# Performance work log

Measured on AMD Instinct MI355X. Metric: run time of the kernel, lower is better.

The kernel has to match this reference:

```python
import jax, jax.numpy as jnp
import numpy as np

D = 1024      # model dim
H = 16        # heads
DH = 64       # dim per head (lucidrains default)
DEPTH = 6
MLP = 2048
P = 32
PD = 3 * P * P   # 3072
NC = 1000
B = 4         # packed sequences
N = 640       # tokens per packed sequence (incl. padding)
M = 18        # images per packed sequence
GRID = 8      # image_size // patch_size
SIZES = [(8,8),(8,8),(7,7),(7,7),(6,8),(8,6),(6,6),(5,7),(7,5),(5,5),(4,8),(8,4),(4,6),(6,4),(4,4),(3,5),(5,3),(3,3)]
SCALE = DH ** -0.5


def _pack_meta():
    hs, ws, ids = [], [], []
    for i, (h, w) in enumerate(SIZES):
        hh, ww = np.meshgrid(np.arange(h), np.arange(w), indexing='ij')
        hs.append(hh.ravel()); ws.append(ww.ravel()); ids.append(np.full(h * w, i))
    h = np.concatenate(hs); w = np.concatenate(ws); ii = np.concatenate(ids)
    pad = N - h.shape[0]
    h = np.pad(h, (0, pad)); w = np.pad(w, (0, pad))
    ii = np.pad(ii, (0, pad), constant_values=-1)  # padding tokens form their own block
    return (np.tile(h, (B, 1)).astype(np.int32),
            np.tile(w, (B, 1)).astype(np.int32),
            np.tile(ii, (B, 1)).astype(np.int32))


def _ln(x, g, b, eps=1e-5):
    m = x.mean(-1, keepdims=True)
    v = ((x - m) ** 2).mean(-1, keepdims=True)
    return (x - m) * jax.lax.rsqrt(v + eps) * g + b


def _heads(t):  # [b, n, H*DH] -> [b, H, n, DH]
    return t.reshape(t.shape[0], t.shape[1], H, DH).swapaxes(1, 2)


def _mha(q_in, kv_in, mask, Wq, Wkv, Wo, qn_g, qn_b, kn_g, kn_b):
    # NaViT attention: pre-norm applied by caller to q_in; per-head qk LayerNorm; no biases.
    q = _ln(_heads(q_in @ Wq), qn_g, qn_b)
    k, v = jnp.split(kv_in @ Wkv, 2, axis=-1)
    k = _ln(_heads(k), kn_g, kn_b)
    v = _heads(v)
    dots = jnp.einsum('bhid,bhjd->bhij', q, k) * SCALE
    dots = jnp.where(mask, dots, jnp.finfo(dots.dtype).min)
    o = jnp.einsum('bhij,bhjd->bhid', jax.nn.softmax(dots, axis=-1), v)
    o = o.swapaxes(1, 2).reshape(o.shape[0], -1, H * DH)
    return o @ Wo


def _forward(patches, pe_ln1_g, pe_ln1_b, W_pe, b_pe, pe_ln2_g, pe_ln2_b, pos_h, pos_w,
             ln1_g, ln1_b, qn_g, qn_b, kn_g, kn_b, Wq, Wkv, Wo, ln2_g, ln2_b,
             W1, b1, W2, b2, fin_g, fin_b, pool_q, pl_ln_g, pl_ln_b, pl_qn_g, pl_qn_b,
             pl_kn_g, pl_kn_b, pl_Wq, pl_Wkv, pl_Wo, head_g, head_b, W_head, b_head,
             h_idx, w_idx, image_ids):
    # patch embedding: LN -> Linear -> LN, then factorized 2D pos embed
    x = _ln(patches, pe_ln1_g, pe_ln1_b) @ W_pe + b_pe
    x = _ln(x, pe_ln2_g, pe_ln2_b)
    x = x + pos_h[h_idx] + pos_w[w_idx]
    # block-diagonal attention mask: tokens attend only within their own image
    blk = (image_ids[:, :, None] == image_ids[:, None, :])[:, None]  # [B,1,N,N]
    for l in range(DEPTH):
        xn = _ln(x, ln1_g[l], ln1_b[l])
        x = x + _mha(xn, xn, blk, Wq[l], Wkv[l], Wo[l], qn_g[l], qn_b[l], kn_g[l], kn_b[l])
        xn = _ln(x, ln2_g[l], ln2_b[l])
        x = x + jax.nn.gelu(xn @ W1[l] + b1[l], approximate=False) @ W2[l] + b2[l]
    x = _ln(x, fin_g, fin_b)
    # attention pooling: one learned query per packed image (context NOT re-normed, as in na_vit)
    queries = jnp.broadcast_to(pool_q, (B, M, D))
    qn = _ln(queries, pl_ln_g, pl_ln_b)
    pmask = (jnp.arange(M)[None, :, None] == image_ids[:, None, :])[:, None]  # [B,1,M,N]
    pooled = _mha(qn, x, pmask, pl_Wq, pl_Wkv, pl_Wo, pl_qn_g, pl_qn_b, pl_kn_g, pl_kn_b) + queries
    pooled = pooled.reshape(B * M, D)
    return _ln(pooled, head_g, head_b) @ W_head + b_head  # [B*M, 1000]


def setup_inputs() -> dict:
    key = jax.random.key(0)
    ks = iter(jax.random.split(key, 32))
    h_idx, w_idx, image_ids = _pack_meta()
    f32 = jnp.float32
    d = dict(
        patches=jax.random.normal(next(ks), (B, N, PD), f32),
        pe_ln1_g=jnp.ones((PD,), f32), pe_ln1_b=jnp.zeros((PD,), f32),
        W_pe=0.02 * jax.random.normal(next(ks), (PD, D), f32), b_pe=jnp.zeros((D,), f32),
        pe_ln2_g=jnp.ones((D,), f32), pe_ln2_b=jnp.zeros((D,), f32),
        pos_h=0.02 * jax.random.normal(next(ks), (GRID, D), f32),
        pos_w=0.02 * jax.random.normal(next(ks), (GRID, D), f32),
        ln1_g=jnp.ones((DEPTH, D), f32), ln1_b=jnp.zeros((DEPTH, D), f32),
        qn_g=jnp.ones((DEPTH, DH), f32), qn_b=jnp.zeros((DEPTH, DH), f32),
        kn_g=jnp.ones((DEPTH, DH), f32), kn_b=jnp.zeros((DEPTH, DH), f32),
        Wq=0.02 * jax.random.normal(next(ks), (DEPTH, D, H * DH), f32),
        Wkv=0.02 * jax.random.normal(next(ks), (DEPTH, D, 2 * H * DH), f32),
        Wo=0.02 * jax.random.normal(next(ks), (DEPTH, H * DH, D), f32),
        ln2_g=jnp.ones((DEPTH, D), f32), ln2_b=jnp.zeros((DEPTH, D), f32),
        W1=0.02 * jax.random.normal(next(ks), (DEPTH, D, MLP), f32), b1=jnp.zeros((DEPTH, MLP), f32),
        W2=0.02 * jax.random.normal(next(ks), (DEPTH, MLP, D), f32), b2=jnp.zeros((DEPTH, D), f32),
        fin_g=jnp.ones((D,), f32), fin_b=jnp.zeros((D,), f32),
        pool_q=0.02 * jax.random.normal(next(ks), (D,), f32),
        pl_ln_g=jnp.ones((D,), f32), pl_ln_b=jnp.zeros((D,), f32),
        pl_qn_g=jnp.ones((DH,), f32), pl_qn_b=jnp.zeros((DH,), f32),
        pl_kn_g=jnp.ones((DH,), f32), pl_kn_b=jnp.zeros((DH,), f32),
        pl_Wq=0.02 * jax.random.normal(next(ks), (D, H * DH), f32),
        pl_Wkv=0.02 * jax.random.normal(next(ks), (D, 2 * H * DH), f32),
        pl_Wo=0.02 * jax.random.normal(next(ks), (H * DH, D), f32),
        head_g=jnp.ones((D,), f32), head_b=jnp.zeros((D,), f32),
        W_head=0.02 * jax.random.normal(next(ks), (D, NC), f32), b_head=jnp.zeros((NC,), f32),
        h_idx=jnp.asarray(h_idx), w_idx=jnp.asarray(w_idx), image_ids=jnp.asarray(image_ids),
    )
    return d


def reference(patches, pe_ln1_g, pe_ln1_b, W_pe, b_pe, pe_ln2_g, pe_ln2_b, pos_h, pos_w,
              ln1_g, ln1_b, qn_g, qn_b, kn_g, kn_b, Wq, Wkv, Wo, ln2_g, ln2_b,
              W1, b1, W2, b2, fin_g, fin_b, pool_q, pl_ln_g, pl_ln_b, pl_qn_g, pl_qn_b,
              pl_kn_g, pl_kn_b, pl_Wq, pl_Wkv, pl_Wo, head_g, head_b, W_head, b_head,
              h_idx, w_idx, image_ids):
    return _forward(patches, pe_ln1_g, pe_ln1_b, W_pe, b_pe, pe_ln2_g, pe_ln2_b, pos_h, pos_w,
                    ln1_g, ln1_b, qn_g, qn_b, kn_g, kn_b, Wq, Wkv, Wo, ln2_g, ln2_b,
                    W1, b1, W2, b2, fin_g, fin_b, pool_q, pl_ln_g, pl_ln_b, pl_qn_g, pl_qn_b,
                    pl_kn_g, pl_kn_b, pl_Wq, pl_Wkv, pl_Wo, head_g, head_b, W_head, b_head,
                    h_idx, w_idx, image_ids)
```

## Files before the change

kernel.cpp:

```cpp
#include <hip/hip_runtime.h>
#include <cmath>

constexpr int kB = 4, kN = 640, kD = 1024, kH = 16, kDH = 64;
constexpr int kDepth = 6, kMLP = 2048, kPD = 3072, kNC = 1000, kM = 18;
constexpr float kScale = 0.125f;
constexpr float kNegInf = -3.4028235e38f;

typedef __bf16 bf16;
typedef __attribute__((ext_vector_type(8))) __bf16 bf16x8;
typedef __attribute__((ext_vector_type(4))) __bf16 bf16x4;
typedef __attribute__((ext_vector_type(4))) float f32x4;

#define AS1 __attribute__((address_space(1)))
#define AS3 __attribute__((address_space(3)))

__device__ __forceinline__ void gload16(const void* g, void* l) {
  __builtin_amdgcn_global_load_lds((AS1 void*)g, (AS3 void*)l, 16, 0, 0);
}

constexpr size_t kMEG = 1048576;
constexpr size_t kOffPe = 0;
constexpr size_t kLayer0 = 3 * kMEG;
constexpr size_t kLayerSz = 8 * kMEG;
constexpr size_t kOffPool = kLayer0 + 6 * kLayerSz;
constexpr size_t kOffPlWq = kOffPool;
constexpr size_t kOffPlWkv = kOffPool + 1 * kMEG;
constexpr size_t kOffPlWo = kOffPool + 3 * kMEG;
constexpr size_t kOffHead = kOffPool + 4 * kMEG;

__global__ __launch_bounds__(256) void wt_all_kernel(
    const float* __restrict__ pe, const float* __restrict__ wq,
    const float* __restrict__ wkv, const float* __restrict__ wo,
    const float* __restrict__ w1, const float* __restrict__ w2,
    const float* __restrict__ plq, const float* __restrict__ plkv,
    const float* __restrict__ plo, const float* __restrict__ whead,
    bf16* __restrict__ WTB) {
  const int j = blockIdx.y;
  const float* W;
  size_t doff;
  int K, Nc, Np;
  if (j == 0) {
    W = pe; K = 3072; Nc = 1024; Np = 1024; doff = kOffPe;
  } else if (j < 31) {
    const int l = (j - 1) / 5, w = (j - 1) % 5;
    const size_t lbase = kLayer0 + (size_t)l * kLayerSz;
    switch (w) {
      case 0:  W = wq  + (size_t)l * kMEG;     K = 1024; Nc = 1024; doff = lbase;            break;
      case 1:  W = wkv + (size_t)l * 2 * kMEG; K = 1024; Nc = 2048; doff = lbase + kMEG;     break;
      case 2:  W = wo  + (size_t)l * kMEG;     K = 1024; Nc = 1024; doff = lbase + 3 * kMEG; break;
      case 3:  W = w1  + (size_t)l * 2 * kMEG; K = 1024; Nc = 2048; doff = lbase + 4 * kMEG; break;
      default: W = w2  + (size_t)l * 2 * kMEG; K = 2048; Nc = 1024; doff = lbase + 6 * kMEG; break;
    }
    Np = Nc;
  } else if (j == 31) { W = plq;  K = 1024; Nc = 1024; Np = 1024; doff = kOffPlWq; }
  else if (j == 32)   { W = plkv; K = 1024; Nc = 2048; Np = 2048; doff = kOffPlWkv; }
  else if (j == 33)   { W = plo;  K = 1024; Nc = 1024; Np = 1024; doff = kOffPlWo; }
  else                { W = whead; K = 1024; Nc = 1000; Np = 1024; doff = kOffHead; }
  const int nb = Np >> 10;
  const int ntiles = nb * (K >> 6);
  const int tile = blockIdx.x;
  if (tile >= ntiles) return;
  const int n0 = (tile % nb) * 1024 + threadIdx.x * 4;
  const int k0 = (tile / nb) * 64;
  const bool inb = (n0 + 3 < Nc);
  bf16* WT = WTB + doff;
#pragma unroll
  for (int ch = 0; ch < 4; ++ch) {
    float4 v[16];
    if (inb) {
      const float* src = W + (size_t)(k0 + ch * 16) * Nc + n0;
#pragma unroll
      for (int i = 0; i < 16; ++i)
        v[i] = *(const float4*)(src + (size_t)i * Nc);
    } else {
#pragma unroll
      for (int i = 0; i < 16; ++i) v[i] = float4{0.f, 0.f, 0.f, 0.f};
    }
#pragma unroll
    for (int c = 0; c < 4; ++c) {
      bf16x8 lo, hi;
#pragma unroll
      for (int i = 0; i < 8; ++i) {
        lo[i] = (bf16)((&v[i].x)[c]);
        hi[i] = (bf16)((&v[i + 8].x)[c]);
      }
      bf16* d = WT + (size_t)(n0 + c) * K + k0 + ch * 16;
      *(bf16x8*)(d) = lo;
      *(bf16x8*)(d + 8) = hi;
    }
  }
}

__global__ __launch_bounds__(64) void span_kernel(
    const int* __restrict__ ids, int2* __restrict__ spans) {
  const int img = blockIdx.x, b = blockIdx.y;
  const int want = (img < kM) ? img : -1;
  int lo = kN, hi = -1;
  for (int j = threadIdx.x; j < kN; j += 64) {
    if (ids[b * kN + j] == want) { lo = min(lo, j); hi = max(hi, j); }
  }
#pragma unroll
  for (int off = 32; off; off >>= 1) {
    lo = min(lo, __shfl_xor(lo, off));
    hi = max(hi, __shfl_xor(hi, off));
  }
  if (threadIdx.x == 0) spans[b * (kM + 1) + img] = make_int2(lo, hi);
}

template <typename OT>
__global__ __launch_bounds__(256) void ln_kernel(
    const float* __restrict__ in, OT* __restrict__ out,
    const float* __restrict__ g, const float* __restrict__ b, int K) {
  const int row = blockIdx.x;
  const float* x = in + (size_t)row * K;
  OT* o = out + (size_t)row * K;
  const int K4 = K >> 2;
  float s = 0.f, s2 = 0.f;
  for (int c = threadIdx.x; c < K4; c += 256) {
    const float4 v = ((const float4*)x)[c];
    s += v.x + v.y + v.z + v.w;
    s2 += v.x * v.x + v.y * v.y + v.z * v.z + v.w * v.w;
  }
#pragma unroll
  for (int off = 32; off; off >>= 1) { s += __shfl_down(s, off); s2 += __shfl_down(s2, off); }
  __shared__ float ls[4], ls2[4];
  __shared__ float sm, sr;
  const int wid = threadIdx.x >> 6, lane = threadIdx.x & 63;
  if (lane == 0) { ls[wid] = s; ls2[wid] = s2; }
  __syncthreads();
  if (threadIdx.x == 0) {
    float a = ls[0] + ls[1] + ls[2] + ls[3];
    float a2 = ls2[0] + ls2[1] + ls2[2] + ls2[3];
    float mean = a / K;
    float var = a2 / K - mean * mean;
    sm = mean; sr = rsqrtf(var + 1e-5f);
  }
  __syncthreads();
  const float mean = sm, r = sr;
  for (int c = threadIdx.x; c < K4; c += 256) {
    const float4 v = ((const float4*)x)[c];
    const float4 gv = ((const float4*)g)[c];
    const float4 bv = ((const float4*)b)[c];
    const int d = c * 4;
    o[d + 0] = (OT)((v.x - mean) * r * gv.x + bv.x);
    o[d + 1] = (OT)((v.y - mean) * r * gv.y + bv.y);
    o[d + 2] = (OT)((v.z - mean) * r * gv.z + bv.z);
    o[d + 3] = (OT)((v.w - mean) * r * gv.w + bv.w);
  }
}

__global__ __launch_bounds__(256) void ln_pos_kernel(
    const float* __restrict__ in, float* __restrict__ out,
    const float* __restrict__ g, const float* __restrict__ b,
    const float* __restrict__ ph, const float* __restrict__ pw,
    const int* __restrict__ hi, const int* __restrict__ wi) {
  const int row = blockIdx.x;
  const float* x = in + (size_t)row * kD;
  float* o = out + (size_t)row * kD;
  const int c = threadIdx.x;
  const float4 v = ((const float4*)x)[c];
  float s = v.x + v.y + v.z + v.w;
  float s2 = v.x * v.x + v.y * v.y + v.z * v.z + v.w * v.w;
#pragma unroll
  for (int off = 32; off; off >>= 1) { s += __shfl_down(s, off); s2 += __shfl_down(s2, off); }
  __shared__ float ls[4], ls2[4];
  __shared__ float sm, sr;
  const int wid = threadIdx.x >> 6, lane = threadIdx.x & 63;
  if (lane == 0) { ls[wid] = s; ls2[wid] = s2; }
  __syncthreads();
  if (threadIdx.x == 0) {
    float a = ls[0] + ls[1] + ls[2] + ls[3];
    float a2 = ls2[0] + ls2[1] + ls2[2] + ls2[3];
    float mean = a / kD;
    float var = a2 / kD - mean * mean;
    sm = mean; sr = rsqrtf(var + 1e-5f);
  }
  __syncthreads();
  const float mean = sm, r = sr;
  const float4* phr = (const float4*)(ph + (size_t)hi[row] * kD);
  const float4* pwr = (const float4*)(pw + (size_t)wi[row] * kD);
  const float4 gv = ((const float4*)g)[c];
  const float4 bv = ((const float4*)b)[c];
  const float4 hv = phr[c], wv = pwr[c];
  float4 ov;
  ov.x = (v.x - mean) * r * gv.x + bv.x + hv.x + wv.x;
  ov.y = (v.y - mean) * r * gv.y + bv.y + hv.y + wv.y;
  ov.z = (v.z - mean) * r * gv.z + bv.z + hv.z + wv.z;
  ov.w = (v.w - mean) * r * gv.w + bv.w + hv.w + wv.w;
  ((float4*)o)[c] = ov;
}

__global__ __launch_bounds__(256) void poolq_kernel(
    const float* __restrict__ pq, const float* __restrict__ lg,
    const float* __restrict__ lb, const bf16* __restrict__ WqT,
    const float* __restrict__ qg, const float* __restrict__ qb,
    float* __restrict__ qpool) {
  const int h = blockIdx.x, tid = threadIdx.x;
  __shared__ float qs[1024];
  __shared__ float red[256];
  __shared__ float ls[4], ls2[4];
  __shared__ float sm, sr;
  const float4 v = ((const float4*)pq)[tid];
  float s = v.x + v.y + v.z + v.w;
  float s2 = v.x * v.x + v.y * v.y + v.z * v.z + v.w * v.w;
#pragma unroll
  for (int off = 32; off; off >>= 1) { s += __shfl_down(s, off); s2 += __shfl_down(s2, off); }
  const int wid = tid >> 6, lane = tid & 63;
  if (lane == 0) { ls[wid] = s; ls2[wid] = s2; }
  __syncthreads();
  if (tid == 0) {
    float a = ls[0] + ls[1] + ls[2] + ls[3];
    float a2 = ls2[0] + ls2[1] + ls2[2] + ls2[3];
    float mean = a / kD;
    sm = mean; sr = rsqrtf(a2 / kD - mean * mean + 1e-5f);
  }
  __syncthreads();
  {
    const float mean = sm, r = sr;
    const float4 gv = ((const float4*)lg)[tid];
    const float4 bv = ((const float4*)lb)[tid];
    qs[tid * 4 + 0] = (v.x - mean) * r * gv.x + bv.x;
    qs[tid * 4 + 1] = (v.y - mean) * r * gv.y + bv.y;
    qs[tid * 4 + 2] = (v.z - mean) * r * gv.z + bv.z;
    qs[tid * 4 + 3] = (v.w - mean) * r * gv.w + bv.w;
  }
  __syncthreads();
  const int d = tid & 63, qq = tid >> 6;
  const bf16* wrow = WqT + (size_t)(h * 64 + d) * 1024 + qq * 256;
  const float* qp = qs + qq * 256;
  float part = 0.f;
  for (int k = 0; k < 256; k += 8) {
    const bf16x8 w8 = *(const bf16x8*)(wrow + k);
#pragma unroll
    for (int e = 0; e < 8; ++e) part += qp[k + e] * (float)w8[e];
  }
  red[tid] = part;
  __syncthreads();
  if (tid < 64) {
    const float dot = red[tid] + red[tid + 64] + red[tid + 128] + red[tid + 192];
    float hs = dot, hs2 = dot * dot;
#pragma unroll
    for (int off = 32; off; off >>= 1) { hs += __shfl_xor(hs, off); hs2 += __shfl_xor(hs2, off); }
    const float m = hs * (1.f / kDH);
    const float r = rsqrtf(hs2 * (1.f / kDH) - m * m + 1e-5f);
    qpool[h * 64 + tid] = (dot - m) * r * qg[tid] + qb[tid];
  }
}

template <int NI, bool OUT_BF, bool GELU, bool HLN>
__global__ __launch_bounds__(256) void gemm64_kernel(
    const bf16* __restrict__ A, const bf16* __restrict__ WT,
    float* __restrict__ Cf, bf16* __restrict__ Cb,
    const float* __restrict__ bias, const float* __restrict__ res,
    const float* __restrict__ hg, const float* __restrict__ hb,
    int K, int Ncol, int nbx) {
  constexpr int BN = NI * 32;
  __shared__ __align__(16) bf16 As[2][64 * 64];
  __shared__ __align__(16) bf16 Bs[2][BN * 64];
  const int tid = threadIdx.x, lane = tid & 63, wid = tid >> 6;
  const int wr = wid >> 1, wc = wid & 1;
  const int cpx = gridDim.x >> 3;
  const int swz = (blockIdx.x & 7) * cpx + (blockIdx.x >> 3);
  const int row0 = (swz / nbx) * 64, col0 = (swz % nbx) * BN;
  const int fr = lane & 15, fg = lane >> 4;
  f32x4 acc[2][NI] = {};
  bf16* sA = As[0]; bf16* sB = Bs[0];
  bf16* dA = As[1]; bf16* dB = Bs[1];

  auto stage = [&](bf16* tA, bf16* tB, int kt) {
#pragma unroll
    for (int i = 0; i < 2; ++i) {
      const int c = i * 256 + tid;
      const int r = c >> 3, ci = c & 7;
      gload16(A + (size_t)(row0 + r) * K + kt + ((ci ^ (r & 7)) * 8),
              tA + (i * 256 + wid * 64) * 8);
    }
#pragma unroll
    for (int i = 0; i < NI; ++i) {
      const int c = i * 256 + tid;
      const int r = c >> 3, ci = c & 7;
      gload16(WT + (size_t)(col0 + r) * K + kt + ((ci ^ (r & 7)) * 8),
              tB + (i * 256 + wid * 64) * 8);
    }
  };
  auto compute = [&](const bf16* tA, const bf16* tB) {
#pragma unroll
    for (int kk = 0; kk < 2; ++kk) {
      bf16x8 af[2], bfr[NI];
#pragma unroll
      for (int mi = 0; mi < 2; ++mi) {
        const int r = wr * 32 + mi * 16 + fr;
        af[mi] = *(const bf16x8*)(tA + r * 64 + (((kk * 4 + fg) ^ (r & 7)) * 8));
      }
#pragma unroll
      for (int ni = 0; ni < NI; ++ni) {
        const int r = wc * (NI * 16) + ni * 16 + fr;
        bfr[ni] = *(const bf16x8*)(tB + r * 64 + (((kk * 4 + fg) ^ (r & 7)) * 8));
      }
#pragma unroll
      for (int mi = 0; mi < 2; ++mi)
#pragma unroll
        for (int ni = 0; ni < NI; ++ni)
          acc[mi][ni] = __builtin_amdgcn_mfma_f32_16x16x32_bf16(af[mi], bfr[ni], acc[mi][ni], 0, 0, 0);
    }
  };

  const int NT = K >> 6;
  stage(sA, sB, 0);
  __syncthreads();
  for (int t = 1; t < NT; ++t) {
    stage(dA, dB, t * 64);
    compute(sA, sB);
    __syncthreads();
    bf16* u;
    u = sA; sA = dA; dA = u;
    u = sB; sB = dB; dB = u;
  }
  compute(sA, sB);

  const int rb = row0 + wr * 32 + fg * 4;
  const int cb = col0 + wc * (NI * 16) + fr;
  float hm[2][4], hr[2][4];
  if (HLN) {
#pragma unroll
    for (int mi = 0; mi < 2; ++mi)
#pragma unroll
      for (int r = 0; r < 4; ++r) {
        float s = 0.f, s2 = 0.f;
#pragma unroll
        for (int ni = 0; ni < NI; ++ni) {
          const float v = acc[mi][ni][r];
          s += v; s2 += v * v;
        }
#pragma unroll
        for (int off = 1; off < 16; off <<= 1) {
          s += __shfl_xor(s, off); s2 += __shfl_xor(s2, off);
        }
        const float m = s * (1.f / kDH);
        hm[mi][r] = m;
        hr[mi][r] = rsqrtf(s2 * (1.f / kDH) - m * m + 1e-5f);
      }
  }
  const bool kHalf = HLN && (cb < kD);
#pragma unroll
  for (int mi = 0; mi < 2; ++mi) {
#pragma unroll
    for (int ni = 0; ni < NI; ++ni) {
      const int cc = cb + ni * 16;
      const float bb = bias ? bias[cc] : 0.f;
      const float hgv = HLN ? hg[ni * 16 + fr] : 0.f;
      const float hbv = HLN ? hb[ni * 16 + fr] : 0.f;
#pragma unroll
      for (int r = 0; r < 4; ++r) {
        const int rr = rb + mi * 16 + r;
        float v = acc[mi][ni][r] + bb;
        if (res) v += res[(size_t)rr * Ncol + cc];
        if (GELU) v = 0.5f * v * (1.f + erff(v * 0.70710678118654752f));
        if (HLN && kHalf) v = (v - hm[mi][r]) * hr[mi][r] * hgv + hbv;
        if (OUT_BF) Cb[(size_t)rr * Ncol + cc] = (bf16)v;
        else        Cf[(size_t)rr * Ncol + cc] = v;
      }
    }
  }
}

template <bool OUT_BF>
__global__ __launch_bounds__(256) void gemm_tail_kernel(
    const bf16* __restrict__ A, const bf16* __restrict__ WT,
    float* __restrict__ Cf, bf16* __restrict__ Cb,
    const float* __restrict__ bias, const float* __restrict__ resv,
    int Mr, int K, int Nc, int ldc, int resmode) {
  __shared__ __align__(16) bf16 As[64][40];
  __shared__ __align__(16) bf16 Bs[128][40];
  const int tid = threadIdx.x;
  const int lane = tid & 63, wid = tid >> 6;
  const int row0 = blockIdx.y * 64, col0 = blockIdx.x * 128;
  f32x4 acc[4][2] = {};
  const int am = tid >> 2, ako = (tid & 3) * 8;
  const int fr = lane & 15, fg = (lane >> 4) * 8;
  for (int k0 = 0; k0 < K; k0 += 32) {
    if (row0 + am < Mr)
      *(bf16x8*)&As[am][ako] = *(const bf16x8*)(A + (size_t)(row0 + am) * K + k0 + ako);
    else {
      bf16x8 z = {};
      *(bf16x8*)&As[am][ako] = z;
    }
#pragma unroll
    for (int it = 0; it < 2; ++it) {
      const int c = it * 256 + tid;
      const int n = c >> 2, ko = (c & 3) * 8;
      *(bf16x8*)&Bs[n][ko] = *(const bf16x8*)(WT + (size_t)(col0 + n) * K + k0 + ko);
    }
    __syncthreads();
    bf16x8 af[4], bfr[2];
#pragma unroll
    for (int mi = 0; mi < 4; ++mi) af[mi] = *(const bf16x8*)&As[mi * 16 + fr][fg];
#pragma unroll
    for (int ni = 0; ni < 2; ++ni) bfr[ni] = *(const bf16x8*)&Bs[wid * 32 + ni * 16 + fr][fg];
#pragma unroll
    for (int mi = 0; mi < 4; ++mi)
#pragma unroll
      for (int ni = 0; ni < 2; ++ni)
        acc[mi][ni] = __builtin_amdgcn_mfma_f32_16x16x32_bf16(af[mi], bfr[ni], acc[mi][ni], 0, 0, 0);
    __syncthreads();
  }
  const int r4 = (lane >> 4) * 4;
  const int cc0 = col0 + wid * 32 + (lane & 15);
#pragma unroll
  for (int mi = 0; mi < 4; ++mi) {
#pragma unroll
    for (int ni = 0; ni < 2; ++ni) {
      const int cc = cc0 + ni * 16;
      if (cc >= Nc) continue;
#pragma unroll
      for (int r = 0; r < 4; ++r) {
        const int rr = row0 + mi * 16 + r4 + r;
        if (rr >= Mr) continue;
        float v = acc[mi][ni][r];
        if (bias) v += bias[cc];
        if (resmode == 1) v += resv[(size_t)rr * ldc + cc];
        else if (resmode == 2) v += resv[cc];
        if (OUT_BF) Cb[(size_t)rr * ldc + cc] = (bf16)v;
        else        Cf[(size_t)rr * ldc + cc] = v;
      }
    }
  }
}

__global__ __launch_bounds__(256) void attn_kernel(
    const bf16* __restrict__ qkv, const int2* __restrict__ spans,
    const float* __restrict__ qg, const float* __restrict__ qb,
    const float* __restrict__ kg, const float* __restrict__ kb,
    bf16* __restrict__ o) {
  const int h = blockIdx.x, img = blockIdx.y, b = blockIdx.z;
  const int tid = threadIdx.x, lane = tid & 63, wid = tid >> 6;
  __shared__ __align__(16) bf16 Qs[64][72];
  __shared__ __align__(16) bf16 Ks[64][72];
  __shared__ __align__(16) bf16 Vt[64][72];
  __shared__ __align__(16) bf16 Ps[64][72];
  const int2 sp = spans[b * (kM + 1) + img];
  if (sp.y < 0) return;
  const int start = sp.x, T = sp.y - sp.x + 1;
  if (img == kM) {
    for (int j = start + wid; j <= sp.y; j += 4)
      o[((size_t)(b * kN + j)) * kD + h * kDH + lane] = (bf16)0.f;
    return;
  }
#pragma unroll
  for (int it = 0; it < 2; ++it) {
    const int ch = it * 256 + tid;
    const int r = ch >> 3, d0 = (ch & 7) * 8;
    if (r < T) {
      const bf16* base = qkv + ((size_t)(b * kN + start + r)) * 3072 + h * kDH + d0;
      const bf16x8 qv = *(const bf16x8*)(base);
      const bf16x8 kv = *(const bf16x8*)(base + 1024);
      const bf16x8 vv = *(const bf16x8*)(base + 2048);
      float qf[8], kf[8];
      float sq = 0.f, sq2 = 0.f, sk = 0.f, sk2 = 0.f;
#pragma unroll
      for (int e = 0; e < 8; ++e) {
        qf[e] = (float)qv[e]; kf[e] = (float)kv[e];
        sq += qf[e]; sq2 += qf[e] * qf[e];
        sk += kf[e]; sk2 += kf[e] * kf[e];
      }
#pragma unroll
      for (int off = 1; off < 8; off <<= 1) {
        sq += __shfl_xor(sq, off); sq2 += __shfl_xor(sq2, off);
        sk += __shfl_xor(sk, off); sk2 += __shfl_xor(sk2, off);
      }
      const float qm = sq * (1.f / 64);
      const float qr = rsqrtf(sq2 * (1.f / 64) - qm * qm + 1e-5f);
      const float km = sk * (1.f / 64);
      const float kr = rsqrtf(sk2 * (1.f / 64) - km * km + 1e-5f);
      bf16x8 qw, kw;
#pragma unroll
      for (int e = 0; e < 8; ++e) {
        qw[e] = (bf16)((qf[e] - qm) * qr * qg[d0 + e] + qb[d0 + e]);
        kw[e] = (bf16)((kf[e] - km) * kr * kg[d0 + e] + kb[d0 + e]);
      }
      *(bf16x8*)&Qs[r][d0] = qw;
      *(bf16x8*)&Ks[r][d0] = kw;
#pragma unroll
      for (int e = 0; e < 8; ++e) Vt[d0 + e][r] = vv[e];
    } else {
      const bf16x8 z = {};
      *(bf16x8*)&Qs[r][d0] = z;
      *(bf16x8*)&Ks[r][d0] = z;
#pragma unroll
      for (int e = 0; e < 8; ++e) Vt[d0 + e][r] = (bf16)0.f;
    }
  }
  __syncthreads();
  const int fr = lane & 15, fg = lane >> 4;
  const int r0 = wid * 16;
  f32x4 sacc[4] = {};
#pragma unroll
  for (int k0 = 0; k0 < 64; k0 += 32) {
    const bf16x8 aq = *(const bf16x8*)&Qs[r0 + fr][k0 + fg * 8];
#pragma unroll
    for (int ni = 0; ni < 4; ++ni) {
      const bf16x8 bk = *(const bf16x8*)&Ks[ni * 16 + fr][k0 + fg * 8];
      sacc[ni] = __builtin_amdgcn_mfma_f32_16x16x32_bf16(aq, bk, sacc[ni], 0, 0, 0);
    }
  }
  float inv[4];
#pragma unroll
  for (int r = 0; r < 4; ++r) {
    float mx = kNegInf;
#pragma unroll
    for (int ni = 0; ni < 4; ++ni) {
      const float s = (ni * 16 + fr < T) ? sacc[ni][r] * kScale : kNegInf;
      sacc[ni][r] = s;
      mx = fmaxf(mx, s);
    }
#pragma unroll
    for (int off = 1; off < 16; off <<= 1) mx = fmaxf(mx, __shfl_xor(mx, off));
    float sum = 0.f;
#pragma unroll
    for (int ni = 0; ni < 4; ++ni) {
      const float p = __expf(sacc[ni][r] - mx);
      sacc[ni][r] = p;
      sum += p;
    }
#pragma unroll
    for (int off = 1; off < 16; off <<= 1) sum += __shfl_xor(sum, off);
    inv[r] = 1.f / sum;
  }
#pragma unroll
  for (int ni = 0; ni < 4; ++ni)
#pragma unroll
    for (int r = 0; r < 4; ++r)
      Ps[r0 + fg * 4 + r][ni * 16 + fr] = (bf16)sacc[ni][r];
  f32x4 oacc[4] = {};
#pragma unroll
  for (int k0 = 0; k0 < 64; k0 += 32) {
    const bf16x8 ap = *(const bf16x8*)&Ps[r0 + fr][k0 + fg * 8];
#pragma unroll
    for (int ni = 0; ni < 4; ++ni) {
      const bf16x8 bv = *(const bf16x8*)&Vt[ni * 16 + fr][k0 + fg * 8];
      oacc[ni] = __builtin_amdgcn_mfma_f32_16x16x32_bf16(ap, bv, oacc[ni], 0, 0, 0);
    }
  }
#pragma unroll
  for (int r = 0; r < 4; ++r) {
    const int i = r0 + fg * 4 + r;
    if (i < T) {
      const size_t orow = ((size_t)(b * kN + start + i)) * kD + h * kDH;
      const float iv = inv[r];
#pragma unroll
      for (int ni = 0; ni < 4; ++ni)
        o[orow + ni * 16 + fr] = (bf16)(oacc[ni][r] * iv);
    }
  }
}

__global__ __launch_bounds__(64) void poolattn_kernel(
    const float* __restrict__ qp, const bf16* __restrict__ kv,
    const int2* __restrict__ spans, bf16* __restrict__ o) {
  const int blk = blockIdx.x;
  const int h = blk % kH;
  const int bm = blk / kH;
  const int m = bm % kM, b = bm / kM;
  const int lane = threadIdx.x;
  __shared__ float sc[kN];
  __shared__ float qs[kDH];
  qs[lane] = qp[h * kDH + lane];
  __syncthreads();
  const int2 sp = spans[b * (kM + 1) + m];
  const int jlo = sp.x, jhi = sp.y + 1;
  float mymax = kNegInf;
  for (int j = jlo + lane; j < jhi; j += 64) {
    const bf16* krow = kv + ((size_t)(b * kN + j)) * (2 * kD) + h * kDH;
    float dot = 0.f;
#pragma unroll
    for (int d = 0; d < kDH; ++d) dot += qs[d] * (float)krow[d];
    const float s = dot * kScale;
    sc[j] = s;
    mymax = fmaxf(mymax, s);
  }
#pragma unroll
  for (int off = 32; off; off >>= 1) mymax = fmaxf(mymax, __shfl_xor(mymax, off));
  float mysum = 0.f;
  for (int j = jlo + lane; j < jhi; j += 64) {
    const float p = __expf(sc[j] - mymax);
    sc[j] = p;
    mysum += p;
  }
#pragma unroll
  for (int off = 32; off; off >>= 1) mysum += __shfl_xor(mysum, off);
  const float inv = 1.f / mysum;
  __syncthreads();
  float acc = 0.f;
  const bf16* vptr = kv + ((size_t)(b * kN + jlo)) * (2 * kD) + kD + h * kDH + lane;
  for (int j = jlo; j < jhi; ++j, vptr += 2 * kD) acc += sc[j] * (float)vptr[0];
  o[((size_t)(b * kM + m)) * kD + h * kDH + lane] = (bf16)(acc * inv);
}

extern "C" void kernel_launch(void* const* d_in, const int* in_sizes, int n_in,
                              void* d_out, int out_size, void* d_ws, size_t ws_size,
                              hipStream_t stream) {
  const float* patches  = (const float*)d_in[0];
  const float* pe_ln1_g = (const float*)d_in[1];
  const float* pe_ln1_b = (const float*)d_in[2];
  const float* W_pe     = (const float*)d_in[3];
  const float* b_pe     = (const float*)d_in[4];
  const float* pe_ln2_g = (const float*)d_in[5];
  const float* pe_ln2_b = (const float*)d_in[6];
  const float* pos_h    = (const float*)d_in[7];
  const float* pos_w    = (const float*)d_in[8];
  const float* ln1_g    = (const float*)d_in[9];
  const float* ln1_b    = (const float*)d_in[10];
  const float* qn_g     = (const float*)d_in[11];
  const float* qn_b     = (const float*)d_in[12];
  const float* kn_g     = (const float*)d_in[13];
  const float* kn_b     = (const float*)d_in[14];
  const float* Wq       = (const float*)d_in[15];
  const float* Wkv      = (const float*)d_in[16];
  const float* Wo       = (const float*)d_in[17];
  const float* ln2_g    = (const float*)d_in[18];
  const float* ln2_b    = (const float*)d_in[19];
  const float* W1       = (const float*)d_in[20];
  const float* b1       = (const float*)d_in[21];
  const float* W2       = (const float*)d_in[22];
  const float* b2       = (const float*)d_in[23];
  const float* fin_g    = (const float*)d_in[24];
  const float* fin_b    = (const float*)d_in[25];
  const float* pool_q   = (const float*)d_in[26];
  const float* pl_ln_g  = (const float*)d_in[27];
  const float* pl_ln_b  = (const float*)d_in[28];
  const float* pl_qn_g  = (const float*)d_in[29];
  const float* pl_qn_b  = (const float*)d_in[30];
  const float* pl_kn_g  = (const float*)d_in[31];
  const float* pl_kn_b  = (const float*)d_in[32];
  const float* pl_Wq    = (const float*)d_in[33];
  const float* pl_Wkv   = (const float*)d_in[34];
  const float* pl_Wo    = (const float*)d_in[35];
  const float* head_g   = (const float*)d_in[36];
  const float* head_b   = (const float*)d_in[37];
  const float* W_head   = (const float*)d_in[38];
  const float* b_head   = (const float*)d_in[39];
  const int* h_idx      = (const int*)d_in[40];
  const int* w_idx      = (const int*)d_in[41];
  const int* image_ids  = (const int*)d_in[42];
  float* out = (float*)d_out;

  const size_t SZ = (size_t)kB * kN * kD;
  char* p = (char*)d_ws;
  float* x    = (float*)p;           p += SZ * 4;
  bf16*  xnb  = (bf16*)p;            p += SZ * 2;
  char*  scratch = p;                p += 32u * 1024 * 1024;
  char*  smalls = p;                 p += 1u * 1024 * 1024;
  bf16*  wtbuf = (bf16*)p;
  bf16*  qkvbb = (bf16*)scratch;
  bf16*  attno = (bf16*)(scratch + 16u * 1024 * 1024);
  bf16*  plnb  = (bf16*)scratch;
  float* emb   = (float*)(scratch + 16u * 1024 * 1024);
  bf16*  h1b   = (bf16*)scratch;
  bf16*  kvpoolb = (bf16*)scratch;
  float* qpool   = (float*)smalls;
  bf16*  opoolb  = (bf16*)(smalls + 8192);
  float* pooled  = (float*)(smalls + 8192 + 163840);
  bf16*  pooledn = (bf16*)(smalls + 8192 + 163840 + 327680);
  int2*  spans   = (int2*)(smalls + 8192 + 163840 + 327680 + 163840);

  const int BN = kB * kN;
  const int nbyM = BN / 64;

  span_kernel<<<dim3(kM + 1, kB), 64, 0, stream>>>(image_ids, spans);
  wt_all_kernel<<<dim3(48, 35), 256, 0, stream>>>(
      W_pe, Wq, Wkv, Wo, W1, W2, pl_Wq, pl_Wkv, pl_Wo, W_head, wtbuf);

  ln_kernel<bf16><<<BN, 256, 0, stream>>>(patches, plnb, pe_ln1_g, pe_ln1_b, kPD);
  gemm64_kernel<2, false, false, false><<<(kD / 64) * nbyM, 256, 0, stream>>>(
      plnb, wtbuf + kOffPe, emb, nullptr, b_pe, nullptr, nullptr, nullptr, kPD, kD, kD / 64);
  ln_pos_kernel<<<BN, 256, 0, stream>>>(emb, x, pe_ln2_g, pe_ln2_b, pos_h, pos_w, h_idx, w_idx);

  for (int l = 0; l < kDepth; ++l) {
    const bf16* lw = wtbuf + kLayer0 + (size_t)l * kLayerSz;
    ln_kernel<bf16><<<BN, 256, 0, stream>>>(x, xnb, ln1_g + (size_t)l * kD, ln1_b + (size_t)l * kD, kD);
    gemm64_kernel<4, true, false, false><<<(3 * kD / 128) * nbyM, 256, 0, stream>>>(
        xnb, lw, nullptr, qkvbb, nullptr, nullptr, nullptr, nullptr, kD, 3 * kD, 3 * kD / 128);
    attn_kernel<<<dim3(kH, kM + 1, kB), 256, 0, stream>>>(
        qkvbb, spans,
        qn_g + (size_t)l * kDH, qn_b + (size_t)l * kDH,
        kn_g + (size_t)l * kDH, kn_b + (size_t)l * kDH, attno);
    gemm64_kernel<2, false, false, false><<<(kD / 64) * nbyM, 256, 0, stream>>>(
        attno, lw + 3 * kMEG, x, nullptr, nullptr, x, nullptr, nullptr, kD, kD, kD / 64);
    ln_kernel<bf16><<<BN, 256, 0, stream>>>(x, xnb, ln2_g + (size_t)l * kD, ln2_b + (size_t)l * kD, kD);
    gemm64_kernel<4, true, true, false><<<(kMLP / 128) * nbyM, 256, 0, stream>>>(
        xnb, lw + 4 * kMEG, nullptr, h1b, b1 + (size_t)l * kMLP, nullptr, nullptr, nullptr, kD, kMLP, kMLP / 128);
    gemm64_kernel<2, false, false, false><<<(kD / 64) * nbyM, 256, 0, stream>>>(
        h1b, lw + 6 * kMEG, x, nullptr, b2 + (size_t)l * kD, x, nullptr, nullptr, kMLP, kD, kD / 64);
  }

  ln_kernel<bf16><<<BN, 256, 0, stream>>>(x, xnb, fin_g, fin_b, kD);

  poolq_kernel<<<kH, 256, 0, stream>>>(
      pool_q, pl_ln_g, pl_ln_b, wtbuf + kOffPlWq, pl_qn_g, pl_qn_b, qpool);
  gemm64_kernel<4, true, false, true><<<(2 * kD / 128) * nbyM, 256, 0, stream>>>(
      xnb, wtbuf + kOffPlWkv, nullptr, kvpoolb, nullptr, nullptr, pl_kn_g, pl_kn_b, kD, 2 * kD, 2 * kD / 128);
  poolattn_kernel<<<kB * kM * kH, 64, 0, stream>>>(qpool, kvpoolb, spans, opoolb);
  gemm_tail_kernel<false><<<dim3(8, 2), 256, 0, stream>>>(
      opoolb, wtbuf + kOffPlWo, pooled, nullptr, nullptr, pool_q, kB * kM, kD, kD, kD, 2);

  ln_kernel<bf16><<<kB * kM, 256, 0, stream>>>(pooled, pooledn, head_g, head_b, kD);
  gemm_tail_kernel<false><<<dim3(8, 2), 256, 0, stream>>>(
      pooledn, wtbuf + kOffHead, out, nullptr, b_head, nullptr, kB * kM, kD, kNC, kNC, 0);
}
```

Before: 1.004 ms.

## Store residual stream in bf16 and retile weight transpose through LDS

The residual stream x moves from fp32 to bf16. The layernorm kernels read bf16 through a new ln_bf_kernel, and the residual GEMMs read and write bf16, which halves the traffic for the residual reads and writes. The weight-transpose kernel is also rewritten to use 64x64 tiles staged in padded shared memory, with many more blocks, so that both the global reads and the writes are coalesced. Accumulating the residual in bf16 across six layers reduces precision and may push the output past the accuracy tolerance.

```diff
diff --git a/kernel.cpp b/kernel.cpp
--- a/kernel.cpp
+++ b/kernel.cpp
@@ -56,38 +56,44 @@
   else if (j == 32)   { W = plkv; K = 1024; Nc = 2048; Np = 2048; doff = kOffPlWkv; }
   else if (j == 33)   { W = plo;  K = 1024; Nc = 1024; Np = 1024; doff = kOffPlWo; }
   else                { W = whead; K = 1024; Nc = 1000; Np = 1024; doff = kOffHead; }
-  const int nb = Np >> 10;
-  const int ntiles = nb * (K >> 6);
+  const int nbx = Np >> 6;
+  const int ntiles = nbx * (K >> 6);
   const int tile = blockIdx.x;
   if (tile >= ntiles) return;
-  const int n0 = (tile % nb) * 1024 + threadIdx.x * 4;
-  const int k0 = (tile / nb) * 64;
-  const bool inb = (n0 + 3 < Nc);
+  const int n0 = (tile % nbx) * 64, k0 = (tile / nbx) * 64;
   bf16* WT = WTB + doff;
-#pragma unroll
-  for (int ch = 0; ch < 4; ++ch) {
-    float4 v[16];
-    if (inb) {
-      const float* src = W + (size_t)(k0 + ch * 16) * Nc + n0;
-#pragma unroll
-      for (int i = 0; i < 16; ++i)
-        v[i] = *(const float4*)(src + (size_t)i * Nc);
-    } else {
-#pragma unroll
-      for (int i = 0; i < 16; ++i) v[i] = float4{0.f, 0.f, 0.f, 0.f};
-    }
-#pragma unroll
-    for (int c = 0; c < 4; ++c) {
-      bf16x8 lo, hi;
-#pragma unroll
-      for (int i = 0; i < 8; ++i) {
-        lo[i] = (bf16)((&v[i].x)[c]);
-        hi[i] = (bf16)((&v[i + 8].x)[c]);
-      }
-      bf16* d = WT + (size_t)(n0 + c) * K + k0 + ch * 16;
-      *(bf16x8*)(d) = lo;
-      *(bf16x8*)(d + 8) = hi;
-    }
+  __shared__ float s[64][65];
+  const int tid = threadIdx.x;
+  if (n0 + 64 <= Nc) {
+#pragma unroll
+    for (int i = 0; i < 4; ++i) {
+      const int c = i * 256 + tid;
+      const int r = c >> 4, cq = c & 15;
+      const float4 v = *(const float4*)(W + (size_t)(k0 + r) * Nc + n0 + cq * 4);
+      s[r][cq * 4 + 0] = v.x; s[r][cq * 4 + 1] = v.y;
+      s[r][cq * 4 + 2] = v.z; s[r][cq * 4 + 3] = v.w;
+    }
+  } else {
+#pragma unroll
+    for (int i = 0; i < 4; ++i) {
+      const int c = i * 256 + tid;
+      const int r = c >> 4, cq = c & 15;
+#pragma unroll
+      for (int e = 0; e < 4; ++e) {
+        const int n = n0 + cq * 4 + e;
+        s[r][cq * 4 + e] = (n < Nc) ? W[(size_t)(k0 + r) * Nc + n] : 0.f;
+      }
+    }
+  }
+  __syncthreads();
+#pragma unroll
+  for (int i = 0; i < 2; ++i) {
+    const int c = i * 256 + tid;
+    const int n = c >> 3, kq = c & 7;
+    bf16x8 w;
+#pragma unroll
+    for (int e = 0; e < 8; ++e) w[e] = (bf16)s[kq * 8 + e][n];
+    *(bf16x8*)(WT + (size_t)(n0 + n) * K + k0 + kq * 8) = w;
   }
 }
 
@@ -149,14 +155,54 @@
   }
 }
 
+__global__ __launch_bounds__(256) void ln_bf_kernel(
+    const bf16* __restrict__ in, bf16* __restrict__ out,
+    const float* __restrict__ g, const float* __restrict__ b) {
+  const int row = blockIdx.x;
+  const bf16* x = in + (size_t)row * kD;
+  bf16* o = out + (size_t)row * kD;
+  const int c = threadIdx.x;
+  const bf16x4 v4 = ((const bf16x4*)x)[c];
+  float f[4];
+  float s = 0.f, s2 = 0.f;
+#pragma unroll
+  for (int e = 0; e < 4; ++e) {
+    f[e] = (float)v4[e];
+    s += f[e]; s2 += f[e] * f[e];
+  }
+#pragma unroll
+  for (int off = 32; off; off >>= 1) { s += __shfl_down(s, off); s2 += __shfl_down(s2, off); }
+  __shared__ float ls[4], ls2[4];
+  __shared__ float sm, sr;
+  const int wid = c >> 6, lane = c & 63;
+  if (lane == 0) { ls[wid] = s; ls2[wid] = s2; }
+  __syncthreads();
+  if (c == 0) {
+    float a = ls[0] + ls[1] + ls[2] + ls[3];
+    float a2 = ls2[0] + ls2[1] + ls2[2] + ls2[3];
+    float mean = a / kD;
+    sm = mean; sr = rsqrtf(a2 / kD - mean * mean + 1e-5f);
+  }
+  __syncthreads();
+  const float mean = sm, r = sr;
+  const float4 gv = ((const float4*)g)[c];
+  const float4 bv = ((const float4*)b)[c];
+  bf16x4 ov;
+  ov[0] = (bf16)((f[0] - mean) * r * gv.x + bv.x);
+  ov[1] = (bf16)((f[1] - mean) * r * gv.y + bv.y);
+  ov[2] = (bf16)((f[2] - mean) * r * gv.z + bv.z);
+  ov[3] = (bf16)((f[3] - mean) * r * gv.w + bv.w);
+  ((bf16x4*)o)[c] = ov;
+}
+
 __global__ __launch_bounds__(256) void ln_pos_kernel(
-    const float* __restrict__ in, float* __restrict__ out,
+    const float* __restrict__ in, bf16* __restrict__ out,
     const float* __restrict__ g, const float* __restrict__ b,
     const float* __restrict__ ph, const float* __restrict__ pw,
     const int* __restrict__ hi, const int* __restrict__ wi) {
   const int row = blockIdx.x;
   const float* x = in + (size_t)row * kD;
-  float* o = out + (size_t)row * kD;
+  bf16* o = out + (size_t)row * kD;
   const int c = threadIdx.x;
   const float4 v = ((const float4*)x)[c];
   float s = v.x + v.y + v.z + v.w;
@@ -182,12 +228,12 @@
   const float4 gv = ((const float4*)g)[c];
   const float4 bv = ((const float4*)b)[c];
   const float4 hv = phr[c], wv = pwr[c];
-  float4 ov;
-  ov.x = (v.x - mean) * r * gv.x + bv.x + hv.x + wv.x;
-  ov.y = (v.y - mean) * r * gv.y + bv.y + hv.y + wv.y;
-  ov.z = (v.z - mean) * r * gv.z + bv.z + hv.z + wv.z;
-  ov.w = (v.w - mean) * r * gv.w + bv.w + hv.w + wv.w;
-  ((float4*)o)[c] = ov;
+  bf16x4 ov;
+  ov[0] = (bf16)((v.x - mean) * r * gv.x + bv.x + hv.x + wv.x);
+  ov[1] = (bf16)((v.y - mean) * r * gv.y + bv.y + hv.y + wv.y);
+  ov[2] = (bf16)((v.z - mean) * r * gv.z + bv.z + hv.z + wv.z);
+  ov[3] = (bf16)((v.w - mean) * r * gv.w + bv.w + hv.w + wv.w);
+  ((bf16x4*)o)[c] = ov;
 }
 
 __global__ __launch_bounds__(256) void poolq_kernel(
@@ -251,7 +297,7 @@
 __global__ __launch_bounds__(256) void gemm64_kernel(
     const bf16* __restrict__ A, const bf16* __restrict__ WT,
     float* __restrict__ Cf, bf16* __restrict__ Cb,
-    const float* __restrict__ bias, const float* __restrict__ res,
+    const float* __restrict__ bias, const bf16* __restrict__ res,
     const float* __restrict__ hg, const float* __restrict__ hb,
     int K, int Ncol, int nbx) {
   constexpr int BN = NI * 32;
@@ -354,7 +400,7 @@
       for (int r = 0; r < 4; ++r) {
         const int rr = rb + mi * 16 + r;
         float v = acc[mi][ni][r] + bb;
-        if (res) v += res[(size_t)rr * Ncol + cc];
+        if (res) v += (float)res[(size_t)rr * Ncol + cc];
         if (GELU) v = 0.5f * v * (1.f + erff(v * 0.70710678118654752f));
         if (HLN && kHalf) v = (v - hm[mi][r]) * hr[mi][r] * hgv + hbv;
         if (OUT_BF) Cb[(size_t)rr * Ncol + cc] = (bf16)v;
@@ -646,7 +692,7 @@
 
   const size_t SZ = (size_t)kB * kN * kD;
   char* p = (char*)d_ws;
-  float* x    = (float*)p;           p += SZ * 4;
+  bf16*  x    = (bf16*)p;            p += SZ * 2;
   bf16*  xnb  = (bf16*)p;            p += SZ * 2;
   char*  scratch = p;                p += 32u * 1024 * 1024;
   char*  smalls = p;                 p += 1u * 1024 * 1024;
@@ -667,7 +713,7 @@
   const int nbyM = BN / 64;
 
   span_kernel<<<dim3(kM + 1, kB), 64, 0, stream>>>(image_ids, spans);
-  wt_all_kernel<<<dim3(48, 35), 256, 0, stream>>>(
+  wt_all_kernel<<<dim3(768, 35), 256, 0, stream>>>(
       W_pe, Wq, Wkv, Wo, W1, W2, pl_Wq, pl_Wkv, pl_Wo, W_head, wtbuf);
 
   ln_kernel<bf16><<<BN, 256, 0, stream>>>(patches, plnb, pe_ln1_g, pe_ln1_b, kPD);
@@ -677,23 +723,23 @@
 
   for (int l = 0; l < kDepth; ++l) {
     const bf16* lw = wtbuf + kLayer0 + (size_t)l * kLayerSz;
-    ln_kernel<bf16><<<BN, 256, 0, stream>>>(x, xnb, ln1_g + (size_t)l * kD, ln1_b + (size_t)l * kD, kD);
+    ln_bf_kernel<<<BN, 256, 0, stream>>>(x, xnb, ln1_g + (size_t)l * kD, ln1_b + (size_t)l * kD);
     gemm64_kernel<4, true, false, false><<<(3 * kD / 128) * nbyM, 256, 0, stream>>>(
         xnb, lw, nullptr, qkvbb, nullptr, nullptr, nullptr, nullptr, kD, 3 * kD, 3 * kD / 128);
     attn_kernel<<<dim3(kH, kM + 1, kB), 256, 0, stream>>>(
         qkvbb, spans,
         qn_g + (size_t)l * kDH, qn_b + (size_t)l * kDH,
         kn_g + (size_t)l * kDH, kn_b + (size_t)l * kDH, attno);
-    gemm64_kernel<2, false, false, false><<<(kD / 64) * nbyM, 256, 0, stream>>>(
-        attno, lw + 3 * kMEG, x, nullptr, nullptr, x, nullptr, nullptr, kD, kD, kD / 64);
-    ln_kernel<bf16><<<BN, 256, 0, stream>>>(x, xnb, ln2_g + (size_t)l * kD, ln2_b + (size_t)l * kD, kD);
+    gemm64_kernel<2, true, false, false><<<(kD / 64) * nbyM, 256, 0, stream>>>(
+        attno, lw + 3 * kMEG, nullptr, x, nullptr, x, nullptr, nullptr, kD, kD, kD / 64);
+    ln_bf_kernel<<<BN, 256, 0, stream>>>(x, xnb, ln2_g + (size_t)l * kD, ln2_b + (size_t)l * kD);
     gemm64_kernel<4, true, true, false><<<(kMLP / 128) * nbyM, 256, 0, stream>>>(
         xnb, lw + 4 * kMEG, nullptr, h1b, b1 + (size_t)l * kMLP, nullptr, nullptr, nullptr, kD, kMLP, kMLP / 128);
-    gemm64_kernel<2, false, false, false><<<(kD / 64) * nbyM, 256, 0, stream>>>(
-        h1b, lw + 6 * kMEG, x, nullptr, b2 + (size_t)l * kD, x, nullptr, nullptr, kMLP, kD, kD / 64);
-  }
-
-  ln_kernel<bf16><<<BN, 256, 0, stream>>>(x, xnb, fin_g, fin_b, kD);
+    gemm64_kernel<2, true, false, false><<<(kD / 64) * nbyM, 256, 0, stream>>>(
+        h1b, lw + 6 * kMEG, nullptr, x, b2 + (size_t)l * kD, x, nullptr, nullptr, kMLP, kD, kD / 64);
+  }
+
+  ln_bf_kernel<<<BN, 256, 0, stream>>>(x, xnb, fin_g, fin_b);
 
   poolq_kernel<<<kH, 256, 0, stream>>>(
       pool_q, pl_ln_g, pl_ln_b, wtbuf + kOffPlWq, pl_qn_g, pl_qn_b, qpool);
```

Result: faster. 941.7 us (median of 2 runs) (-6.2%).
